# Kernel tuning notes

Hardware: AMD Instinct MI355X
Metric: run time of the kernel (lower is better)

The kernel has to match this reference:

```python
import jax, jax.numpy as jnp
import numpy as np

# ---- static config (mirrors Net.__init__) ----
N_NODES, N_EDGES = 4000, 20000
N_PROTS, D = 919, 512            # node_emb: Embedding(919, 512); F_in = D (divide_input=False)
TOWERS, F_OUT = 4, D // 4        # F_out = out_channels // towers = 128
EDGE_D = 50
N_GRAPHS, N_CLASSES = 32, 10
N_LAYERS = 2
EPS_BN, EPS_STD = 1e-5, 1e-5

# deg histogram passed to PNAConv; only avg_deg['log'] matters for the scalers used
DEG_HIST = np.array([0., 800., 1200., 900., 600., 300., 150., 50.])
AVG_DEG_LOG = float((np.log(np.arange(DEG_HIST.size) + 1.0) * DEG_HIST).sum() / DEG_HIST.sum())


def setup_inputs() -> dict:
    key = jax.random.key(0)
    ks = jax.random.split(key, 16)
    g = lambda i, shape, s=0.05: (jax.random.normal(ks[i], shape, jnp.float32) * s)
    return dict(
        node_emb_w=g(0, (N_PROTS, D), 0.1),
        edge_emb_w=g(1, (2, EDGE_D), 0.1),
        pe_w=g(2, (2, D)), pe_b=jnp.zeros((D,), jnp.float32),
        edge_enc_w=g(3, (N_LAYERS, EDGE_D, D)), edge_enc_b=jnp.zeros((N_LAYERS, D), jnp.float32),
        pre_w=g(4, (N_LAYERS, TOWERS, 3 * D, D)), pre_b=jnp.zeros((N_LAYERS, TOWERS, D), jnp.float32),
        post_w=g(5, (N_LAYERS, TOWERS, 13 * D, F_OUT)), post_b=jnp.zeros((N_LAYERS, TOWERS, F_OUT), jnp.float32),
        lin_w=g(6, (N_LAYERS, D, D)), lin_b=jnp.zeros((N_LAYERS, D), jnp.float32),
        bn_gamma=jnp.ones((N_LAYERS, D), jnp.float32), bn_beta=jnp.zeros((N_LAYERS, D), jnp.float32),
        acts=jax.random.normal(ks[7], (N_NODES, 2), jnp.float32),
        fc1_w=g(8, (D, 2 * D)), fc1_b=jnp.zeros((2 * D,), jnp.float32),
        fc_out_w=g(9, (2 * D, N_CLASSES)), fc_out_b=jnp.zeros((N_CLASSES,), jnp.float32),
        prelu_a=jnp.float32(0.25),
        global_idx=jax.random.randint(ks[10], (N_NODES,), 0, N_PROTS),
        sign=jax.random.randint(ks[11], (N_EDGES,), 0, 2),
        edge_index=jax.random.randint(ks[12], (2, N_EDGES), 0, N_NODES),
        batch=jnp.sort(jax.random.randint(ks[13], (N_NODES,), 0, N_GRAPHS)),
    )


def _pna_layer(x, src, dst, e, pre_w, pre_b, post_w, post_b, lin_w, lin_b):
    # x: [N, D], e: [E, D] (edge_encoder output), pre_w: [T, 3D, D], post_w: [T, 13D, F_OUT]
    N, E = x.shape[0], src.shape[0]
    # pre-NN on cat([x_i, x_j, edge_attr]) expressed as split matmuls (pre_layers=1 -> single Linear)
    Wi, Wj, We = pre_w[:, :D], pre_w[:, D:2 * D], pre_w[:, 2 * D:]
    m = (jnp.einsum('ef,tfd->etd', x[dst], Wi)
         + jnp.einsum('ef,tfd->etd', x[src], Wj)
         + jnp.einsum('ef,tfd->etd', e, We) + pre_b)          # [E, T, D]
    # multi-aggregation at destination nodes: mean / min / max / std
    cnt = jax.ops.segment_sum(jnp.ones((E,), m.dtype), dst, N)  # in-degree
    has = (cnt > 0)[:, None, None]
    deg = jnp.maximum(cnt, 1.0)[:, None, None]                  # clamp(1) as in PyG
    s1 = jax.ops.segment_sum(m, dst, N)
    s2 = jax.ops.segment_sum(m * m, dst, N)
    mean = s1 / deg
    std = jnp.sqrt(jax.nn.relu(s2 / deg - mean * mean) + EPS_STD)
    mn = jnp.where(has, jax.ops.segment_min(m, dst, N), 0.0)
    mx = jnp.where(has, jax.ops.segment_max(m, dst, N), 0.0)
    agg = jnp.concatenate([mean, mn, mx, std], axis=-1)         # [N, T, 4D]
    # degree scalers: identity, amplification, attenuation
    amp = jnp.log(deg + 1.0) / AVG_DEG_LOG
    out = jnp.concatenate([agg, agg * amp, agg / amp], axis=-1)  # [N, T, 12D]
    # post-NN on cat([x, out]) as split matmuls (post_layers=1)
    Wx, Wo = post_w[:, :D], post_w[:, D:]
    o = (jnp.einsum('nf,tfd->ntd', x, Wx)
         + jnp.einsum('ntf,tfd->ntd', out, Wo) + post_b)        # [N, T, F_OUT]
    return o.reshape(N, TOWERS * F_OUT) @ lin_w + lin_b         # [N, D]


def reference(node_emb_w, edge_emb_w, pe_w, pe_b, edge_enc_w, edge_enc_b,
              pre_w, pre_b, post_w, post_b, lin_w, lin_b, bn_gamma, bn_beta,
              acts, fc1_w, fc1_b, fc_out_w, fc_out_b, prelu_a,
              global_idx, sign, edge_index, batch):
    src, dst = edge_index[0], edge_index[1]
    x = node_emb_w[global_idx] + (acts @ pe_w + pe_b)           # node_emb + PostEncoding
    ea = edge_emb_w[sign]                                       # [E, 50]
    for l in range(N_LAYERS):
        e = ea @ edge_enc_w[l] + edge_enc_b[l]                  # shared edge encoder
        h = _pna_layer(x, src, dst, e, pre_w[l], pre_b[l], post_w[l], post_b[l], lin_w[l], lin_b[l])
        mu = h.mean(axis=0)
        var = ((h - mu) ** 2).mean(axis=0)                      # training-mode BatchNorm (biased var)
        x = jax.nn.relu(bn_gamma[l] * (h - mu) * jax.lax.rsqrt(var + EPS_BN) + bn_beta[l])
    pooled = jax.ops.segment_sum(x, batch, N_GRAPHS)            # global_add_pool
    z = pooled @ fc1_w + fc1_b
    z = jnp.where(z > 0, z, prelu_a * z)                        # PReLU
    logits = z @ fc_out_w + fc_out_b
    return jax.nn.log_softmax(logits, axis=-1)
```

## Files before the change

### kernel.cpp

```cpp
#include <hip/hip_runtime.h>
#include <hip/hip_bf16.h>
#include <float.h>

#define NN 4000
#define NE 20000
#define DD 512
#define NT 4
#define FO 128
#define NG 32
#define NC 10
#define XGW 4608
#define AVGLOG 1.2548916493836102f
#define EPS_STD_ 1e-5f
#define EPS_BN_ 1e-5f

typedef __bf16 bf16x8 __attribute__((ext_vector_type(8)));
typedef float  f32x4  __attribute__((ext_vector_type(4)));

__device__ __forceinline__ void async_copy16(const void* g, void* l) {
    __builtin_amdgcn_global_load_lds((const __attribute__((address_space(1))) void*)g,
                                     (__attribute__((address_space(3))) void*)l, 16, 0, 0);
}

template<int OUT_BF16, int HAS_BIAS>
__device__ __forceinline__ void core64(
    const __bf16* __restrict__ A, int lda,
    const __bf16* __restrict__ BT, int ldbt,
    void* __restrict__ Cv, int ldc,
    const float* __restrict__ bias,
    int M, int K, int m0, int n0)
{
    __shared__ __bf16 As[64 * 32];
    __shared__ __bf16 Bs[128 * 32];
    const int tid = threadIdx.x;
    const int wave = tid >> 6, lane = tid & 63;
    const int wr = wave >> 1, wc = wave & 1;
    const int fr = lane & 15, fq = lane >> 4;
    f32x4 acc[2][4];
    const f32x4 zero = {0.f, 0.f, 0.f, 0.f};
#pragma unroll
    for (int i = 0; i < 2; ++i)
#pragma unroll
        for (int j = 0; j < 4; ++j) acc[i][j] = zero;

    const int ar = tid >> 2, akc = (tid & 3) * 8;
    int arow = m0 + ar; if (arow > M - 1) arow = M - 1;
    for (int k0 = 0; k0 < K; k0 += 32) {
        async_copy16(A + (size_t)arow * lda + k0 + akc, As + tid * 8);
#pragma unroll
        for (int i = 0; i < 2; ++i) {
            const int cb = tid + 256 * i;
            const int br = cb >> 2, bkc = (cb & 3) * 8;
            async_copy16(BT + (size_t)(n0 + br) * ldbt + k0 + bkc, Bs + cb * 8);
        }
        __syncthreads();
        bf16x8 a[2], b[4];
#pragma unroll
        for (int mi = 0; mi < 2; ++mi) a[mi] = *(const bf16x8*)(As + (wr * 32 + mi * 16 + fr) * 32 + fq * 8);
#pragma unroll
        for (int ni = 0; ni < 4; ++ni) b[ni] = *(const bf16x8*)(Bs + (wc * 64 + ni * 16 + fr) * 32 + fq * 8);
#pragma unroll
        for (int mi = 0; mi < 2; ++mi)
#pragma unroll
            for (int ni = 0; ni < 4; ++ni)
                acc[mi][ni] = __builtin_amdgcn_mfma_f32_16x16x32_bf16(a[mi], b[ni], acc[mi][ni], 0, 0, 0);
        __syncthreads();
    }
    float* Cf = (float*)Cv; __bf16* Cb = (__bf16*)Cv;
#pragma unroll
    for (int mi = 0; mi < 2; ++mi) {
#pragma unroll
        for (int ni = 0; ni < 4; ++ni) {
            const int col = n0 + wc * 64 + ni * 16 + fr;
            const int rb = m0 + wr * 32 + mi * 16 + fq * 4;
            const float bv = HAS_BIAS ? bias[col] : 0.f;
#pragma unroll
            for (int r = 0; r < 4; ++r) {
                const int rowc = rb + r;
                if (rowc < M) {
                    const float v = acc[mi][ni][r] + bv;
                    if (OUT_BF16) Cb[(size_t)rowc * ldc + col] = (__bf16)v;
                    else          Cf[(size_t)rowc * ldc + col] = v;
                }
            }
        }
    }
}

__global__ __launch_bounds__(256) void k_xg(const __bf16* __restrict__ XB, const __bf16* __restrict__ WCAT,
                                            __bf16* __restrict__ XG) {
    core64<1, 0>(XB, 512, WCAT, 512, XG, XGW, nullptr, NN, 512,
                 blockIdx.y * 64, blockIdx.x * 128);
}

__global__ __launch_bounds__(256) void k_gw(const __bf16* __restrict__ AB, const __bf16* __restrict__ WTT,
                                            float* __restrict__ GWP) {
    const int t = blockIdx.z & 3, kh = blockIdx.z >> 2;
    const __bf16* A  = AB  + (size_t)t * 2048 + (size_t)kh * 1024;
    const __bf16* BT = WTT + (size_t)t * 384 * 2048 + (size_t)kh * 1024;
    float* C = GWP + (size_t)blockIdx.z * NN * 384;
    core64<0, 0>(A, 8192, BT, 2048, C, 384, nullptr, NN, 1024,
                 blockIdx.y * 64, blockIdx.x * 128);
}

__global__ void k_combine(const __bf16* __restrict__ XG, const float* __restrict__ GWP,
                          const float* __restrict__ amp, const float* __restrict__ ramp,
                          const float* __restrict__ pb, __bf16* __restrict__ OB,
                          float* __restrict__ BN, float* __restrict__ PL, int zero_pl) {
    const int idx = blockIdx.x * 256 + threadIdx.x;
    const int n = idx >> 9, c = idx & 511;
    const int t = c >> 7, o = c & 127;
    const float* ga = GWP + ((size_t)t) * NN * 384 + (size_t)n * 384;
    const float* gb = GWP + ((size_t)(4 + t)) * NN * 384 + (size_t)n * 384;
    const float w1 = ga[o] + gb[o];
    const float w2 = ga[128 + o] + gb[128 + o];
    const float w3 = ga[256 + o] + gb[256 + o];
    const float gx = (float)XG[(size_t)n * XGW + 4096 + c];
    const float v = gx + w1 + amp[n] * w2 + ramp[n] * w3 + pb[c];
    OB[idx] = (__bf16)v;
    if (blockIdx.x == 0) {
        const int tid = threadIdx.x;
        BN[tid] = 0.f; BN[256 + tid] = 0.f; BN[512 + tid] = 0.f; BN[768 + tid] = 0.f;
        if (zero_pl)
            for (int i = tid; i < NG * DD; i += 256) PL[i] = 0.f;
    }
}

__global__ __launch_bounds__(256) void k_lin(const __bf16* __restrict__ OB, const __bf16* __restrict__ WLINT,
                                             const float* __restrict__ bl, float* __restrict__ H,
                                             float* __restrict__ BN) {
    const int n0c = blockIdx.x * 128, m0 = blockIdx.y * 64;
    __shared__ __bf16 As[64 * 32];
    __shared__ __bf16 Bs[128 * 32];
    __shared__ float bnS[128], bnQ[128];
    const int tid = threadIdx.x;
    if (tid < 128) { bnS[tid] = 0.f; bnQ[tid] = 0.f; }
    const int wave = tid >> 6, lane = tid & 63;
    const int wr = wave >> 1, wc = wave & 1;
    const int fr = lane & 15, fq = lane >> 4;
    f32x4 acc[2][4];
    const f32x4 zero = {0.f, 0.f, 0.f, 0.f};
#pragma unroll
    for (int i = 0; i < 2; ++i)
#pragma unroll
        for (int j = 0; j < 4; ++j) acc[i][j] = zero;

    const int ar = tid >> 2, akc = (tid & 3) * 8;
    int arow = m0 + ar; if (arow > NN - 1) arow = NN - 1;
    for (int k0 = 0; k0 < 512; k0 += 32) {
        async_copy16(OB + (size_t)arow * 512 + k0 + akc, As + tid * 8);
#pragma unroll
        for (int i = 0; i < 2; ++i) {
            const int cb = tid + 256 * i;
            const int br = cb >> 2, bkc = (cb & 3) * 8;
            async_copy16(WLINT + (size_t)(n0c + br) * 512 + k0 + bkc, Bs + cb * 8);
        }
        __syncthreads();
        bf16x8 a[2], b[4];
#pragma unroll
        for (int mi = 0; mi < 2; ++mi) a[mi] = *(const bf16x8*)(As + (wr * 32 + mi * 16 + fr) * 32 + fq * 8);
#pragma unroll
        for (int ni = 0; ni < 4; ++ni) b[ni] = *(const bf16x8*)(Bs + (wc * 64 + ni * 16 + fr) * 32 + fq * 8);
#pragma unroll
        for (int mi = 0; mi < 2; ++mi)
#pragma unroll
            for (int ni = 0; ni < 4; ++ni)
                acc[mi][ni] = __builtin_amdgcn_mfma_f32_16x16x32_bf16(a[mi], b[ni], acc[mi][ni], 0, 0, 0);
        __syncthreads();
    }
#pragma unroll
    for (int ni = 0; ni < 4; ++ni) {
        const int lc = wc * 64 + ni * 16 + fr;
        const int col = n0c + lc;
        const float bv = bl[col];
        float s = 0.f, q = 0.f;
#pragma unroll
        for (int mi = 0; mi < 2; ++mi) {
#pragma unroll
            for (int r = 0; r < 4; ++r) {
                const int rowc = m0 + wr * 32 + mi * 16 + fq * 4 + r;
                if (rowc < NN) {
                    const float v = acc[mi][ni][r] + bv;
                    H[(size_t)rowc * 512 + col] = v;
                    s += v; q += v * v;
                }
            }
        }
        atomicAdd(&bnS[lc], s); atomicAdd(&bnQ[lc], q);
    }
    __syncthreads();
    if (tid < 128) {
        atomicAdd(&BN[n0c + tid], bnS[tid]);
        atomicAdd(&BN[512 + n0c + tid], bnQ[tid]);
    }
}

__device__ __forceinline__ void tr32(const float* __restrict__ S, int sld,
                                     __bf16* __restrict__ D, int dld, int tx, int ty) {
    __shared__ float t[32][33];
    const int y0 = ty * 4;
#pragma unroll
    for (int i = 0; i < 4; ++i) t[y0 + i][tx] = S[(size_t)(y0 + i) * sld + tx];
    __syncthreads();
#pragma unroll
    for (int i = 0; i < 4; ++i) D[(size_t)(y0 + i) * dld + tx] = (__bf16)t[tx][y0 + i];
}

__global__ __launch_bounds__(256) void k_tr(const float* __restrict__ pw, const float* __restrict__ pow_,
                                            const float* __restrict__ lw,
                                            const float* __restrict__ eemb, const float* __restrict__ eew,
                                            const float* __restrict__ eeb, const float* __restrict__ pb,
                                            __bf16* __restrict__ WCAT, __bf16* __restrict__ WTT,
                                            __bf16* __restrict__ WLINT, float* __restrict__ EM) {
    const int id = blockIdx.x;
    const int tx = threadIdx.x & 31, ty = threadIdx.x >> 5;
    if (id < 2048) {
        const int z = id >> 8, r = id & 255;
        const int t = z & 3, half = z >> 2;
        const int x = r & 15, y = r >> 4;
        const float* S = pw + ((size_t)(t * 1536 + half * 512 + y * 32)) * 512 + x * 32;
        __bf16* D = WCAT + ((size_t)(half * 2048 + t * 512 + x * 32)) * 512 + y * 32;
        tr32(S, 512, D, 512, tx, ty);
    } else if (id < 2304) {
        const int id3 = id - 2048;
        const int t = id3 >> 6, r = id3 & 63;
        const int x = r & 3, y = r >> 2;
        const float* S = pow_ + ((size_t)(t * 6656 + y * 32)) * 128 + x * 32;
        __bf16* D = WCAT + ((size_t)(4096 + t * 128 + x * 32)) * 512 + y * 32;
        tr32(S, 128, D, 512, tx, ty);
    } else if (id < 5376) {
        const int id4 = id - 2304;
        const int z = id4 >> 8, r = id4 & 255;
        const int t = z / 3, w = z % 3;
        const int x = r & 3, y = r >> 2;
        const float* S = pow_ + ((size_t)(t * 6656 + 512 + w * 2048 + y * 32)) * 128 + x * 32;
        __bf16* D = WTT + (size_t)t * 384 * 2048 + ((size_t)(w * 128 + x * 32)) * 2048 + y * 32;
        tr32(S, 128, D, 2048, tx, ty);
    } else if (id < 5632) {
        const int r = id - 5376;
        const int x = r & 15, y = r >> 4;
        const float* S = lw + (size_t)y * 32 * 512 + x * 32;
        __bf16* D = WLINT + (size_t)x * 32 * 512 + y * 32;
        tr32(S, 512, D, 512, tx, ty);
    } else {
        __shared__ float eks[512];
        __shared__ float part[4][64];
        const int tid = threadIdx.x;
        const int id5 = id - 5632;
        const int k = id5 >> 5;
        const int g0 = (id5 & 31) * 64;
#pragma unroll
        for (int h = 0; h < 2; ++h) {
            const int f = tid + h * 256;
            float s = eeb[f];
            for (int c = 0; c < 50; ++c) s += eemb[k * 50 + c] * eew[(size_t)c * 512 + f];
            eks[f] = s;
        }
        __syncthreads();
        const int wave = tid >> 6, lane = tid & 63;
        const int g = g0 + lane;
        const int t = g >> 9, d = g & 511;
        const float* Wp = pw + ((size_t)(t * 1536 + 1024)) * 512 + d;
        float s = 0.f;
        const int f0 = wave * 128;
#pragma unroll 4
        for (int f = f0; f < f0 + 128; ++f) s += eks[f] * Wp[(size_t)f * 512];
        part[wave][lane] = s;
        __syncthreads();
        if (tid < 64) {
            const int gg = g0 + tid;
            EM[k * 2048 + gg] = pb[gg] + part[0][tid] + part[1][tid] + part[2][tid] + part[3][tid];
        }
    }
}

__global__ void k_count(const int* __restrict__ dst, int* __restrict__ cnt) {
    int e = blockIdx.x * 256 + threadIdx.x;
    if (e < NE) atomicAdd(&cnt[dst[e]], 1);
}

__global__ __launch_bounds__(1024) void k_scan_bx(const int* __restrict__ cnt, int* __restrict__ offs,
                                                  float* __restrict__ amp, float* __restrict__ ramp,
                                                  const float* __restrict__ nemb, const float* __restrict__ acts,
                                                  const float* __restrict__ pew, const float* __restrict__ peb,
                                                  const int* __restrict__ gidx, __bf16* __restrict__ XB) {
    const int t = threadIdx.x;
    if (blockIdx.x == 0) {
        __shared__ int part[1024];
        const int base = t * 4;
        int loc[4]; int s = 0;
#pragma unroll
        for (int i = 0; i < 4; ++i) { int v = (base + i < NN) ? cnt[base + i] : 0; loc[i] = s; s += v; }
        part[t] = s;
        __syncthreads();
        for (int o = 1; o < 1024; o <<= 1) {
            int v = (t >= o) ? part[t - o] : 0;
            __syncthreads();
            part[t] += v;
            __syncthreads();
        }
        const int pre = (t > 0) ? part[t - 1] : 0;
#pragma unroll
        for (int i = 0; i < 4; ++i) if (base + i < NN) offs[base + i] = pre + loc[i];
        if (t == 1023) offs[NN] = part[1023];
        for (int n = t; n < NN; n += 1024) {
            float deg = fmaxf((float)cnt[n], 1.0f);
            float a = logf(deg + 1.0f) / AVGLOG;
            amp[n] = a; ramp[n] = 1.0f / a;
        }
    } else {
        const int idx = (blockIdx.x - 1) * 1024 + t;
        const int n = idx >> 9, d = idx & 511;
        float v = nemb[(size_t)gidx[n] * DD + d] + acts[n * 2] * pew[d] + acts[n * 2 + 1] * pew[DD + d] + peb[d];
        XB[idx] = (__bf16)v;
    }
}

__global__ void k_fill(const int* __restrict__ src, const int* __restrict__ dst,
                       const int* __restrict__ sgn, const int* __restrict__ offs,
                       int* __restrict__ fill, int* __restrict__ esrc, int* __restrict__ esgn) {
    int e = blockIdx.x * 256 + threadIdx.x;
    if (e < NE) {
        int d = dst[e];
        int pos = offs[d] + atomicAdd(&fill[d], 1);
        esrc[pos] = src[e];
        esgn[pos] = sgn[e];
    }
}

__global__ __launch_bounds__(256) void k_agg(const __bf16* __restrict__ XG, const float* __restrict__ EM,
                                             const int* __restrict__ offs, const int* __restrict__ cnt,
                                             const int* __restrict__ esrc, const int* __restrict__ esgn,
                                             __bf16* __restrict__ AB) {
    const int n = blockIdx.x;
    const int g = threadIdx.x * 8;
    float xid[8], em0[8], em1[8];
    {
        bf16x8 xb = *(const bf16x8*)(XG + (size_t)n * XGW + g);
#pragma unroll
        for (int i = 0; i < 8; ++i) xid[i] = (float)xb[i];
    }
    *(float4*)&em0[0] = *(const float4*)&EM[g];
    *(float4*)&em0[4] = *(const float4*)&EM[g + 4];
    *(float4*)&em1[0] = *(const float4*)&EM[2048 + g];
    *(float4*)&em1[4] = *(const float4*)&EM[2048 + g + 4];
    float s1[8], s2[8], mn[8], mx[8];
#pragma unroll
    for (int i = 0; i < 8; ++i) { s1[i] = 0.f; s2[i] = 0.f; mn[i] = FLT_MAX; mx[i] = -FLT_MAX; }
    const int j0 = offs[n], j1 = offs[n + 1];
    for (int j = j0; j < j1; ++j) {
        const int s = esrc[j];
        const int sg = esgn[j];
        bf16x8 xv = *(const bf16x8*)(XG + (size_t)s * XGW + 2048 + g);
#pragma unroll
        for (int i = 0; i < 8; ++i) {
            float m = xid[i] + (float)xv[i] + (sg ? em1[i] : em0[i]);
            s1[i] += m; s2[i] += m * m;
            mn[i] = fminf(mn[i], m); mx[i] = fmaxf(mx[i], m);
        }
    }
    const int c = cnt[n];
    const float deg = fmaxf((float)c, 1.0f);
    const float rdeg = 1.0f / deg;
    bf16x8 vmean, vmn, vmx, vsd;
#pragma unroll
    for (int i = 0; i < 8; ++i) {
        float mean = s1[i] * rdeg;
        float var = s2[i] * rdeg - mean * mean;
        float sd = sqrtf(fmaxf(var, 0.f) + EPS_STD_);
        float mnv = (c == 0) ? 0.f : mn[i];
        float mxv = (c == 0) ? 0.f : mx[i];
        vmean[i] = (__bf16)mean; vmn[i] = (__bf16)mnv; vmx[i] = (__bf16)mxv; vsd[i] = (__bf16)sd;
    }
    const int t = g >> 9, d = g & 511;
    __bf16* base = AB + (size_t)n * 8192 + (size_t)t * 2048 + d;
    *(bf16x8*)(base + 0 * DD) = vmean;
    *(bf16x8*)(base + 1 * DD) = vmn;
    *(bf16x8*)(base + 2 * DD) = vmx;
    *(bf16x8*)(base + 3 * DD) = vsd;
}

__global__ void k_bnapply(const float* __restrict__ H, const float* __restrict__ BN,
                          const float* __restrict__ gamma, const float* __restrict__ beta,
                          __bf16* __restrict__ XB, float* __restrict__ PL,
                          const int* __restrict__ batch, int last) {
    int idx = blockIdx.x * 256 + threadIdx.x;
    int n = idx >> 9, d = idx & 511;
    float mu = BN[d] * (1.0f / NN);
    float var = BN[512 + d] * (1.0f / NN) - mu * mu;
    float v = gamma[d] * (H[idx] - mu) * rsqrtf(var + EPS_BN_) + beta[d];
    v = fmaxf(v, 0.f);
    if (last) atomicAdd(&PL[(size_t)batch[n] * DD + d], v);
    else XB[idx] = (__bf16)v;
}

__global__ __launch_bounds__(128) void k_fc1(const float* __restrict__ PL, const float* __restrict__ W1,
                                             const float* __restrict__ b1, const float* __restrict__ pa,
                                             float* __restrict__ Z) {
    const int g = blockIdx.x >> 3;
    const int j = (blockIdx.x & 7) * 128 + threadIdx.x;
    __shared__ float pl[512];
    for (int i = threadIdx.x; i < 512; i += 128) pl[i] = PL[(size_t)g * 512 + i];
    __syncthreads();
    const float* w = W1 + j;
    float s0 = 0.f, s1 = 0.f, s2 = 0.f, s3 = 0.f;
#pragma unroll 2
    for (int f = 0; f < 512; f += 4) {
        s0 += pl[f + 0] * w[(size_t)(f + 0) * 1024];
        s1 += pl[f + 1] * w[(size_t)(f + 1) * 1024];
        s2 += pl[f + 2] * w[(size_t)(f + 2) * 1024];
        s3 += pl[f + 3] * w[(size_t)(f + 3) * 1024];
    }
    float s = b1[j] + ((s0 + s1) + (s2 + s3));
    const float a = *pa;
    Z[(size_t)g * 1024 + j] = s > 0.f ? s : a * s;
}

__global__ __launch_bounds__(64) void k_out(const float* __restrict__ Z, const float* __restrict__ Wo,
                                            const float* __restrict__ bo, float* __restrict__ out) {
    const int g = blockIdx.x, t = threadIdx.x;
    float part[NC];
#pragma unroll
    for (int c = 0; c < NC; ++c) part[c] = 0.f;
    for (int f = t; f < 1024; f += 64) {
        const float zv = Z[(size_t)g * 1024 + f];
#pragma unroll
        for (int c = 0; c < NC; ++c) part[c] += zv * Wo[(size_t)f * NC + c];
    }
#pragma unroll
    for (int off = 32; off > 0; off >>= 1)
#pragma unroll
        for (int c = 0; c < NC; ++c) part[c] += __shfl_down(part[c], off);
    if (t == 0) {
        float lg[NC], mxv = -FLT_MAX;
#pragma unroll
        for (int c = 0; c < NC; ++c) { lg[c] = part[c] + bo[c]; mxv = fmaxf(mxv, lg[c]); }
        float se = 0.f;
#pragma unroll
        for (int c = 0; c < NC; ++c) se += expf(lg[c] - mxv);
        const float lse = mxv + logf(se);
#pragma unroll
        for (int c = 0; c < NC; ++c) out[g * NC + c] = lg[c] - lse;
    }
}

extern "C" void kernel_launch(void* const* d_in, const int* in_sizes, int n_in,
                              void* d_out, int out_size, void* d_ws, size_t ws_size,
                              hipStream_t stream) {
    const float* node_emb_w = (const float*)d_in[0];
    const float* edge_emb_w = (const float*)d_in[1];
    const float* pe_w   = (const float*)d_in[2];
    const float* pe_b   = (const float*)d_in[3];
    const float* edge_enc_w = (const float*)d_in[4];
    const float* edge_enc_b = (const float*)d_in[5];
    const float* pre_w  = (const float*)d_in[6];
    const float* pre_b  = (const float*)d_in[7];
    const float* post_w = (const float*)d_in[8];
    const float* post_b = (const float*)d_in[9];
    const float* lin_w  = (const float*)d_in[10];
    const float* lin_b  = (const float*)d_in[11];
    const float* bn_gamma = (const float*)d_in[12];
    const float* bn_beta  = (const float*)d_in[13];
    const float* acts   = (const float*)d_in[14];
    const float* fc1_w  = (const float*)d_in[15];
    const float* fc1_b  = (const float*)d_in[16];
    const float* fc_out_w = (const float*)d_in[17];
    const float* fc_out_b = (const float*)d_in[18];
    const float* prelu_a  = (const float*)d_in[19];
    const int* global_idx = (const int*)d_in[20];
    const int* sgn        = (const int*)d_in[21];
    const int* edge_index = (const int*)d_in[22];
    const int* batch      = (const int*)d_in[23];
    float* out = (float*)d_out;

    char* W = (char*)d_ws;
    size_t off = 0;
    auto alloc = [&](size_t bytes) { void* p = W + off; off += (bytes + 63) & ~(size_t)63; return p; };
    __bf16* XB    = (__bf16*)alloc((size_t)NN * DD * 2);
    float*  H     = (float*)alloc((size_t)NN * DD * 4);
    __bf16* XG    = (__bf16*)alloc((size_t)NN * XGW * 2);
    __bf16* AB    = (__bf16*)alloc((size_t)NN * 8192 * 2);
    float*  GWP   = (float*)alloc((size_t)8 * NN * 384 * 4);
    __bf16* OB    = (__bf16*)alloc((size_t)NN * DD * 2);
    __bf16* WCAT  = (__bf16*)alloc((size_t)XGW * 512 * 2);
    __bf16* WTT   = (__bf16*)alloc((size_t)NT * 384 * 2048 * 2);
    __bf16* WLINT = (__bf16*)alloc((size_t)512 * 512 * 2);
    float*  EM    = (float*)alloc(2 * 2048 * 4);
    float*  BN    = (float*)alloc(1024 * 4);
    float*  PL    = (float*)alloc((size_t)NG * DD * 4);
    float*  ZB    = (float*)alloc((size_t)NG * 1024 * 4);
    float*  AMP   = (float*)alloc(NN * 4);
    float*  RAMP  = (float*)alloc(NN * 4);
    int*    CNT   = (int*)alloc(NN * 4);
    int*    FILL  = (int*)alloc(NN * 4);
    int*    OFFS  = (int*)alloc((NN + 1) * 4);
    int*    ESRC  = (int*)alloc(NE * 4);
    int*    ESGN  = (int*)alloc(NE * 4);

    const int* src = edge_index;
    const int* dst = edge_index + NE;

    hipMemsetAsync(CNT, 0, 2 * NN * sizeof(int), stream);
    k_count<<<(NE + 255) / 256, 256, 0, stream>>>(dst, CNT);
    k_scan_bx<<<2001, 1024, 0, stream>>>(CNT, OFFS, AMP, RAMP,
                                         node_emb_w, acts, pe_w, pe_b, global_idx, XB);
    k_fill<<<(NE + 255) / 256, 256, 0, stream>>>(src, dst, sgn, OFFS, FILL, ESRC, ESGN);

    for (int l = 0; l < 2; ++l) {
        const float* pre_w_l  = pre_w  + (size_t)l * NT * 3 * DD * DD;
        const float* pre_b_l  = pre_b  + (size_t)l * NT * DD;
        const float* post_w_l = post_w + (size_t)l * NT * 6656 * FO;
        const float* post_b_l = post_b + (size_t)l * NT * FO;
        const float* lin_w_l  = lin_w  + (size_t)l * DD * DD;
        const float* lin_b_l  = lin_b  + (size_t)l * DD;
        const float* eew_l    = edge_enc_w + (size_t)l * 50 * DD;
        const float* eeb_l    = edge_enc_b + (size_t)l * DD;

        k_tr<<<5696, 256, 0, stream>>>(pre_w_l, post_w_l, lin_w_l,
                                       edge_emb_w, eew_l, eeb_l, pre_b_l,
                                       WCAT, WTT, WLINT, EM);
        k_xg<<<dim3(36, 63), 256, 0, stream>>>(XB, WCAT, XG);
        k_agg<<<NN, 256, 0, stream>>>(XG, EM, OFFS, CNT, ESRC, ESGN, AB);
        k_gw<<<dim3(3, 63, 8), 256, 0, stream>>>(AB, WTT, GWP);
        k_combine<<<NN * DD / 256, 256, 0, stream>>>(XG, GWP, AMP, RAMP, post_b_l, OB, BN, PL, l == 1);
        k_lin<<<dim3(4, 63), 256, 0, stream>>>(OB, WLINT, lin_b_l, H, BN);
        k_bnapply<<<NN * DD / 256, 256, 0, stream>>>(H, BN, bn_gamma + (size_t)l * DD,
                                                     bn_beta + (size_t)l * DD, XB, PL, batch, l == 1);
    }

    k_fc1<<<256, 128, 0, stream>>>(PL, fc1_w, fc1_b, prelu_a, ZB);
    k_out<<<NG, 64, 0, stream>>>(ZB, fc_out_w, fc_out_b, out);
}
```

Before: 553.7 us.

## Fuse combine into GEMM epilogues with atomic accumulation and larger 128x128 tiles

Removes the k_combine kernel and the 8-slice GWP fp32 buffer. k_xg now writes the x-part of the post output (plus bias) straight into an fp32 OF buffer. k_gw scales its partials by amp/ramp and atomically adds them into OF. Both GEMMs move to 128x128 block tiles with 4x4 MFMA fragments per wave, and k_lin now reads fp32 OF and converts it to bf16 in registers. This saves a large intermediate write and read plus one launch, in exchange for many fp32 atomics and a non-deterministic summation order.

```diff
diff --git a/kernel.cpp b/kernel.cpp
--- a/kernel.cpp
+++ b/kernel.cpp
@@ -9,7 +9,7 @@
 #define FO 128
 #define NG 32
 #define NC 10
-#define XGW 4608
+#define XGW 4096
 #define AVGLOG 1.2548916493836102f
 #define EPS_STD_ 1e-5f
 #define EPS_BN_ 1e-5f
@@ -22,111 +22,149 @@
                                      (__attribute__((address_space(3))) void*)l, 16, 0, 0);
 }
 
-template<int OUT_BF16, int HAS_BIAS>
-__device__ __forceinline__ void core64(
-    const __bf16* __restrict__ A, int lda,
-    const __bf16* __restrict__ BT, int ldbt,
-    void* __restrict__ Cv, int ldc,
-    const float* __restrict__ bias,
-    int M, int K, int m0, int n0)
-{
-    __shared__ __bf16 As[64 * 32];
+__global__ __launch_bounds__(256) void k_xg(const __bf16* __restrict__ XB, const __bf16* __restrict__ WCAT,
+                                            const float* __restrict__ pb,
+                                            __bf16* __restrict__ XG, float* __restrict__ OF,
+                                            float* __restrict__ BN, float* __restrict__ PL, int zero_pl) {
+    const int m0 = blockIdx.y * 128, n0 = blockIdx.x * 128;
+    __shared__ __bf16 As[128 * 32];
     __shared__ __bf16 Bs[128 * 32];
     const int tid = threadIdx.x;
     const int wave = tid >> 6, lane = tid & 63;
-    const int wr = wave >> 1, wc = wave & 1;
+    const int wm = (wave >> 1) * 64, wn = (wave & 1) * 64;
     const int fr = lane & 15, fq = lane >> 4;
-    f32x4 acc[2][4];
+    const int fk = fq * 8;
+    const int srow = lane >> 2, skc = (lane & 3) * 8;
+
+    f32x4 acc[4][4];
     const f32x4 zero = {0.f, 0.f, 0.f, 0.f};
 #pragma unroll
-    for (int i = 0; i < 2; ++i)
+    for (int i = 0; i < 4; ++i)
 #pragma unroll
         for (int j = 0; j < 4; ++j) acc[i][j] = zero;
 
-    const int ar = tid >> 2, akc = (tid & 3) * 8;
-    int arow = m0 + ar; if (arow > M - 1) arow = M - 1;
-    for (int k0 = 0; k0 < K; k0 += 32) {
-        async_copy16(A + (size_t)arow * lda + k0 + akc, As + tid * 8);
-#pragma unroll
-        for (int i = 0; i < 2; ++i) {
-            const int cb = tid + 256 * i;
-            const int br = cb >> 2, bkc = (cb & 3) * 8;
-            async_copy16(BT + (size_t)(n0 + br) * ldbt + k0 + bkc, Bs + cb * 8);
-        }
-        __syncthreads();
-        bf16x8 a[2], b[4];
-#pragma unroll
-        for (int mi = 0; mi < 2; ++mi) a[mi] = *(const bf16x8*)(As + (wr * 32 + mi * 16 + fr) * 32 + fq * 8);
-#pragma unroll
-        for (int ni = 0; ni < 4; ++ni) b[ni] = *(const bf16x8*)(Bs + (wc * 64 + ni * 16 + fr) * 32 + fq * 8);
-#pragma unroll
-        for (int mi = 0; mi < 2; ++mi)
+    for (int k0 = 0; k0 < 512; k0 += 32) {
+#pragma unroll
+        for (int q = 0; q < 2; ++q) {
+            const int row = wave * 32 + q * 16 + srow;
+            int ar = m0 + row; if (ar > NN - 1) ar = NN - 1;
+            async_copy16(XB + (size_t)ar * 512 + k0 + skc, As + wave * 1024 + q * 512);
+            async_copy16(WCAT + (size_t)(n0 + row) * 512 + k0 + skc, Bs + wave * 1024 + q * 512);
+        }
+        __syncthreads();
+        bf16x8 af[4], bfr[4];
+#pragma unroll
+        for (int mi = 0; mi < 4; ++mi) af[mi]  = *(const bf16x8*)(As + (wm + mi * 16 + fr) * 32 + fk);
+#pragma unroll
+        for (int ni = 0; ni < 4; ++ni) bfr[ni] = *(const bf16x8*)(Bs + (wn + ni * 16 + fr) * 32 + fk);
+#pragma unroll
+        for (int mi = 0; mi < 4; ++mi)
 #pragma unroll
             for (int ni = 0; ni < 4; ++ni)
-                acc[mi][ni] = __builtin_amdgcn_mfma_f32_16x16x32_bf16(a[mi], b[ni], acc[mi][ni], 0, 0, 0);
-        __syncthreads();
-    }
-    float* Cf = (float*)Cv; __bf16* Cb = (__bf16*)Cv;
-#pragma unroll
-    for (int mi = 0; mi < 2; ++mi) {
-#pragma unroll
-        for (int ni = 0; ni < 4; ++ni) {
-            const int col = n0 + wc * 64 + ni * 16 + fr;
-            const int rb = m0 + wr * 32 + mi * 16 + fq * 4;
-            const float bv = HAS_BIAS ? bias[col] : 0.f;
-#pragma unroll
-            for (int r = 0; r < 4; ++r) {
-                const int rowc = rb + r;
-                if (rowc < M) {
-                    const float v = acc[mi][ni][r] + bv;
-                    if (OUT_BF16) Cb[(size_t)rowc * ldc + col] = (__bf16)v;
-                    else          Cf[(size_t)rowc * ldc + col] = v;
+                acc[mi][ni] = __builtin_amdgcn_mfma_f32_16x16x32_bf16(af[mi], bfr[ni], acc[mi][ni], 0, 0, 0);
+        __syncthreads();
+    }
+    if (n0 < 4096) {
+#pragma unroll
+        for (int mi = 0; mi < 4; ++mi) {
+#pragma unroll
+            for (int ni = 0; ni < 4; ++ni) {
+                const int col = n0 + wn + ni * 16 + fr;
+                const int rb = m0 + wm + mi * 16 + fq * 4;
+#pragma unroll
+                for (int r = 0; r < 4; ++r) {
+                    const int rowc = rb + r;
+                    if (rowc < NN) XG[(size_t)rowc * XGW + col] = (__bf16)acc[mi][ni][r];
                 }
             }
         }
-    }
-}
-
-__global__ __launch_bounds__(256) void k_xg(const __bf16* __restrict__ XB, const __bf16* __restrict__ WCAT,
-                                            __bf16* __restrict__ XG) {
-    core64<1, 0>(XB, 512, WCAT, 512, XG, XGW, nullptr, NN, 512,
-                 blockIdx.y * 64, blockIdx.x * 128);
-}
-
-__global__ __launch_bounds__(256) void k_gw(const __bf16* __restrict__ AB, const __bf16* __restrict__ WTT,
-                                            float* __restrict__ GWP) {
-    const int t = blockIdx.z & 3, kh = blockIdx.z >> 2;
-    const __bf16* A  = AB  + (size_t)t * 2048 + (size_t)kh * 1024;
-    const __bf16* BT = WTT + (size_t)t * 384 * 2048 + (size_t)kh * 1024;
-    float* C = GWP + (size_t)blockIdx.z * NN * 384;
-    core64<0, 0>(A, 8192, BT, 2048, C, 384, nullptr, NN, 1024,
-                 blockIdx.y * 64, blockIdx.x * 128);
-}
-
-__global__ void k_combine(const __bf16* __restrict__ XG, const float* __restrict__ GWP,
-                          const float* __restrict__ amp, const float* __restrict__ ramp,
-                          const float* __restrict__ pb, __bf16* __restrict__ OB,
-                          float* __restrict__ BN, float* __restrict__ PL, int zero_pl) {
-    const int idx = blockIdx.x * 256 + threadIdx.x;
-    const int n = idx >> 9, c = idx & 511;
-    const int t = c >> 7, o = c & 127;
-    const float* ga = GWP + ((size_t)t) * NN * 384 + (size_t)n * 384;
-    const float* gb = GWP + ((size_t)(4 + t)) * NN * 384 + (size_t)n * 384;
-    const float w1 = ga[o] + gb[o];
-    const float w2 = ga[128 + o] + gb[128 + o];
-    const float w3 = ga[256 + o] + gb[256 + o];
-    const float gx = (float)XG[(size_t)n * XGW + 4096 + c];
-    const float v = gx + w1 + amp[n] * w2 + ramp[n] * w3 + pb[c];
-    OB[idx] = (__bf16)v;
-    if (blockIdx.x == 0) {
-        const int tid = threadIdx.x;
+    } else {
+        const int ocb = n0 - 4096;
+#pragma unroll
+        for (int mi = 0; mi < 4; ++mi) {
+#pragma unroll
+            for (int ni = 0; ni < 4; ++ni) {
+                const int oc = ocb + wn + ni * 16 + fr;
+                const float bv = pb[oc];
+                const int rb = m0 + wm + mi * 16 + fq * 4;
+#pragma unroll
+                for (int r = 0; r < 4; ++r) {
+                    const int rowc = rb + r;
+                    if (rowc < NN) OF[(size_t)rowc * 512 + oc] = acc[mi][ni][r] + bv;
+                }
+            }
+        }
+    }
+    if (blockIdx.x == 32 && blockIdx.y == 0) {
         BN[tid] = 0.f; BN[256 + tid] = 0.f; BN[512 + tid] = 0.f; BN[768 + tid] = 0.f;
         if (zero_pl)
             for (int i = tid; i < NG * DD; i += 256) PL[i] = 0.f;
     }
 }
 
-__global__ __launch_bounds__(256) void k_lin(const __bf16* __restrict__ OB, const __bf16* __restrict__ WLINT,
+__global__ __launch_bounds__(256) void k_gw(const __bf16* __restrict__ AB, const __bf16* __restrict__ WTT,
+                                            const float* __restrict__ amp, const float* __restrict__ ramp,
+                                            float* __restrict__ OF) {
+    const int t = blockIdx.z & 3, kh = blockIdx.z >> 2;
+    const int xg = blockIdx.x;
+    const int m0 = blockIdx.y * 128;
+    const __bf16* A  = AB  + (size_t)t * 2048 + (size_t)kh * 1024;
+    const __bf16* BT = WTT + (size_t)t * 384 * 2048 + (size_t)xg * 128 * 2048 + (size_t)kh * 1024;
+    __shared__ __bf16 As[128 * 32];
+    __shared__ __bf16 Bs[128 * 32];
+    const int tid = threadIdx.x;
+    const int wave = tid >> 6, lane = tid & 63;
+    const int wm = (wave >> 1) * 64, wn = (wave & 1) * 64;
+    const int fr = lane & 15, fq = lane >> 4;
+    const int fk = fq * 8;
+    const int srow = lane >> 2, skc = (lane & 3) * 8;
+
+    f32x4 acc[4][4];
+    const f32x4 zero = {0.f, 0.f, 0.f, 0.f};
+#pragma unroll
+    for (int i = 0; i < 4; ++i)
+#pragma unroll
+        for (int j = 0; j < 4; ++j) acc[i][j] = zero;
+
+    for (int k0 = 0; k0 < 1024; k0 += 32) {
+#pragma unroll
+        for (int q = 0; q < 2; ++q) {
+            const int row = wave * 32 + q * 16 + srow;
+            int ar = m0 + row; if (ar > NN - 1) ar = NN - 1;
+            async_copy16(A + (size_t)ar * 8192 + k0 + skc, As + wave * 1024 + q * 512);
+            async_copy16(BT + (size_t)row * 2048 + k0 + skc, Bs + wave * 1024 + q * 512);
+        }
+        __syncthreads();
+        bf16x8 af[4], bfr[4];
+#pragma unroll
+        for (int mi = 0; mi < 4; ++mi) af[mi]  = *(const bf16x8*)(As + (wm + mi * 16 + fr) * 32 + fk);
+#pragma unroll
+        for (int ni = 0; ni < 4; ++ni) bfr[ni] = *(const bf16x8*)(Bs + (wn + ni * 16 + fr) * 32 + fk);
+#pragma unroll
+        for (int mi = 0; mi < 4; ++mi)
+#pragma unroll
+            for (int ni = 0; ni < 4; ++ni)
+                acc[mi][ni] = __builtin_amdgcn_mfma_f32_16x16x32_bf16(af[mi], bfr[ni], acc[mi][ni], 0, 0, 0);
+        __syncthreads();
+    }
+#pragma unroll
+    for (int mi = 0; mi < 4; ++mi) {
+        const int rb = m0 + wm + mi * 16 + fq * 4;
+#pragma unroll
+        for (int r = 0; r < 4; ++r) {
+            const int row = rb + r;
+            if (row < NN) {
+                const float w = (xg == 0) ? 1.0f : (xg == 1 ? amp[row] : ramp[row]);
+                float* orow = OF + (size_t)row * 512 + t * 128;
+#pragma unroll
+                for (int ni = 0; ni < 4; ++ni)
+                    atomicAdd(orow + wn + ni * 16 + fr, acc[mi][ni][r] * w);
+            }
+        }
+    }
+}
+
+__global__ __launch_bounds__(256) void k_lin(const float* __restrict__ OF, const __bf16* __restrict__ WLINT,
                                              const float* __restrict__ bl, float* __restrict__ H,
                                              float* __restrict__ BN) {
     const int n0c = blockIdx.x * 128, m0 = blockIdx.y * 64;
@@ -147,8 +185,14 @@
 
     const int ar = tid >> 2, akc = (tid & 3) * 8;
     int arow = m0 + ar; if (arow > NN - 1) arow = NN - 1;
+    const float* asrc = OF + (size_t)arow * 512;
     for (int k0 = 0; k0 < 512; k0 += 32) {
-        async_copy16(OB + (size_t)arow * 512 + k0 + akc, As + tid * 8);
+        float4 f0 = *(const float4*)(asrc + k0 + akc);
+        float4 f1 = *(const float4*)(asrc + k0 + akc + 4);
+        bf16x8 av;
+        av[0] = (__bf16)f0.x; av[1] = (__bf16)f0.y; av[2] = (__bf16)f0.z; av[3] = (__bf16)f0.w;
+        av[4] = (__bf16)f1.x; av[5] = (__bf16)f1.y; av[6] = (__bf16)f1.z; av[7] = (__bf16)f1.w;
+        *(bf16x8*)(As + ar * 32 + akc) = av;
 #pragma unroll
         for (int i = 0; i < 2; ++i) {
             const int cb = tid + 256 * i;
@@ -480,9 +524,8 @@
     float*  H     = (float*)alloc((size_t)NN * DD * 4);
     __bf16* XG    = (__bf16*)alloc((size_t)NN * XGW * 2);
     __bf16* AB    = (__bf16*)alloc((size_t)NN * 8192 * 2);
-    float*  GWP   = (float*)alloc((size_t)8 * NN * 384 * 4);
-    __bf16* OB    = (__bf16*)alloc((size_t)NN * DD * 2);
-    __bf16* WCAT  = (__bf16*)alloc((size_t)XGW * 512 * 2);
+    float*  OF    = (float*)alloc((size_t)NN * DD * 4);
+    __bf16* WCAT  = (__bf16*)alloc((size_t)4608 * 512 * 2);
     __bf16* WTT   = (__bf16*)alloc((size_t)NT * 384 * 2048 * 2);
     __bf16* WLINT = (__bf16*)alloc((size_t)512 * 512 * 2);
     float*  EM    = (float*)alloc(2 * 2048 * 4);
@@ -519,11 +562,10 @@
         k_tr<<<5696, 256, 0, stream>>>(pre_w_l, post_w_l, lin_w_l,
                                        edge_emb_w, eew_l, eeb_l, pre_b_l,
                                        WCAT, WTT, WLINT, EM);
-        k_xg<<<dim3(36, 63), 256, 0, stream>>>(XB, WCAT, XG);
+        k_xg<<<dim3(36, 32), 256, 0, stream>>>(XB, WCAT, post_b_l, XG, OF, BN, PL, l == 1);
         k_agg<<<NN, 256, 0, stream>>>(XG, EM, OFFS, CNT, ESRC, ESGN, AB);
-        k_gw<<<dim3(3, 63, 8), 256, 0, stream>>>(AB, WTT, GWP);
-        k_combine<<<NN * DD / 256, 256, 0, stream>>>(XG, GWP, AMP, RAMP, post_b_l, OB, BN, PL, l == 1);
-        k_lin<<<dim3(4, 63), 256, 0, stream>>>(OB, WLINT, lin_b_l, H, BN);
+        k_gw<<<dim3(3, 32, 8), 256, 0, stream>>>(AB, WTT, AMP, RAMP, OF);
+        k_lin<<<dim3(4, 63), 256, 0, stream>>>(OF, WLINT, lin_b_l, H, BN);
         k_bnapply<<<NN * DD / 256, 256, 0, stream>>>(H, BN, bn_gamma + (size_t)l * DD,
                                                      bn_beta + (size_t)l * DD, XB, PL, batch, l == 1);
     }
```

After: 566.5 us. 2.3% more time.
